# Kernel tuning notes

Hardware: AMD Instinct MI355X
Metric: run time of the kernel (lower is better)

Reference implementation:

```python
import jax, jax.numpy as jnp
import numpy as np

K = 1024          # num_embeddings
D = 256           # embedding_dim
BETA = 0.25       # commitment_cost
DECAY = 0.99
EPS = 1e-05
N = 65536         # number of tokens


def setup_inputs() -> dict:
    key = jax.random.key(0)
    k1, k2, k3 = jax.random.split(key, 3)
    inputs = jax.random.normal(k1, (N, D), dtype=jnp.float32)
    # codebook initialized uniform(-1/K, 1/K) as in torch init
    codebook = jax.random.uniform(k2, (K, D), dtype=jnp.float32, minval=-1.0 / K, maxval=1.0 / K)
    ema_cluster_size = jnp.zeros((K,), dtype=jnp.float32)
    ema_w = codebook  # _ema_w initialized to a clone of the weights
    return {"inputs": inputs, "codebook": codebook,
            "ema_cluster_size": ema_cluster_size, "ema_w": ema_w}


def reference(inputs, codebook, ema_cluster_size, ema_w):
    flat = inputs.reshape(-1, D)  # [N, D]
    # squared L2 distances to every codebook entry: [N, K]
    distances = (jnp.sum(flat * flat, axis=1, keepdims=True)
                 + jnp.sum(codebook * codebook, axis=1)
                 - 2.0 * jnp.matmul(flat, codebook.T))
    encoding_indices = jnp.argmin(distances, axis=1)          # [N]
    quantized = codebook[encoding_indices].reshape(inputs.shape)  # gather

    # EMA codebook update (training branch). one-hot^T @ flat == segment_sum.
    counts = jax.ops.segment_sum(jnp.ones((flat.shape[0],), flat.dtype),
                                 encoding_indices, num_segments=K)  # [K]
    dw = jax.ops.segment_sum(flat, encoding_indices, num_segments=K)  # [K, D]
    new_cs = DECAY * ema_cluster_size + (1.0 - DECAY) * counts
    n_total = jnp.sum(new_cs)
    new_cs = (new_cs + EPS) / (n_total + K * EPS) * n_total
    new_ema_w = DECAY * ema_w + (1.0 - DECAY) * dw
    new_weight = new_ema_w / new_cs[:, None]

    commitment_loss = jnp.mean((quantized - inputs) ** 2)
    vq_loss = BETA * commitment_loss
    quantized_st = inputs + jax.lax.stop_gradient(quantized - inputs)

    avg_probs = counts / flat.shape[0]
    perplexity = jnp.exp(-jnp.sum(avg_probs * jnp.log(avg_probs + 1e-10)))

    return (quantized_st, vq_loss, encoding_indices, perplexity,
            new_cs, new_ema_w, new_weight)
```

## Files before the change

kernel.cpp:

```cpp
#include <hip/hip_runtime.h>
#include <math.h>

#define KC 1024
#define DD 256
#define NT 65536
#define MARGIN 2.5e-4f
#define HCAP 4096

#define W_COUNTS 0
#define W_LOSS   1024
#define W_HCNT   1025
#define W_CNORM  1028
#define W_OFFS   2052
#define W_CUR    3076
#define W_HLIST  4100
#define W_SORT   8196
#define W_IDX    73732
#define W_DWB    139268
#define W_AMIN   401412
#define W_CCAT   409604
#define W_CBT    540676
#define W_XH     802820

typedef _Float16 h8 __attribute__((ext_vector_type(8)));
typedef _Float16 h4 __attribute__((ext_vector_type(4)));
typedef float f32x4 __attribute__((ext_vector_type(4)));
typedef unsigned long long u64;

__device__ __forceinline__ void gl_lds16(const _Float16* g, _Float16* l) {
    __builtin_amdgcn_global_load_lds(
        (const __attribute__((address_space(1))) unsigned int*)g,
        (__attribute__((address_space(3))) unsigned int*)l, 16, 0, 0);
}

__device__ __forceinline__ void merge2(float& v1, float& i1, float& v2,
                                       float b1, float bi, float b2) {
    if (b1 < v1) { v2 = fminf(v1, b2); v1 = b1; i1 = bi; }
    else         { v2 = fminf(v2, b1); }
}

__device__ __forceinline__ int physrow(int row, int d) {
    return ((((row >> 2) ^ ((d >> 2) & 7)) << 2) | (row & 3));
}

__global__ __launch_bounds__(256) void vq_prepx(const float* __restrict__ X,
                                                _Float16* __restrict__ Xcat) {
    int gid = blockIdx.x * 256 + threadIdx.x;
    float4 v = reinterpret_cast<const float4*>(X)[gid];
    int n = gid >> 6, d = (gid & 63) << 2;
    h4 hi;
    hi[0] = (_Float16)v.x; hi[1] = (_Float16)v.y;
    hi[2] = (_Float16)v.z; hi[3] = (_Float16)v.w;
    *(h4*)(Xcat + (size_t)n * 256 + d) = hi;
}

__global__ __launch_bounds__(64) void vq_prep(const float* __restrict__ cb,
                                              _Float16* __restrict__ Ccat,
                                              float* __restrict__ cnorm,
                                              float* __restrict__ cbT) {
    const int k = blockIdx.x;
    const int l = threadIdx.x;
    float4 v = reinterpret_cast<const float4*>(cb)[k * 64 + l];
    cbT[(4 * l + 0) * KC + k] = v.x;
    cbT[(4 * l + 1) * KC + k] = v.y;
    cbT[(4 * l + 2) * KC + k] = v.z;
    cbT[(4 * l + 3) * KC + k] = v.w;
    h4 hi;
    hi[0] = (_Float16)(v.x * 16384.0f); hi[1] = (_Float16)(v.y * 16384.0f);
    hi[2] = (_Float16)(v.z * 16384.0f); hi[3] = (_Float16)(v.w * 16384.0f);
    *(h4*)(Ccat + (size_t)k * 256 + 4 * l) = hi;
    float s = v.x * v.x + v.y * v.y + v.z * v.z + v.w * v.w;
    #pragma unroll
    for (int off = 32; off; off >>= 1) s += __shfl_down(s, off, 64);
    if (l == 0) cnorm[k] = s;
}

__global__ __launch_bounds__(256) void vq_screen(
        const _Float16* __restrict__ Xcat, const _Float16* __restrict__ Ccat,
        const float* __restrict__ cnorm, float* __restrict__ counts,
        int* __restrict__ idxw, float* __restrict__ idxf,
        int* __restrict__ hardCnt, int* __restrict__ hardList) {
    __shared__ _Float16 As[8192];
    __shared__ _Float16 Bs[8192];
    __shared__ float wbuf[2][128][3];
    const int t = threadIdx.x;
    const int lane = t & 63, w = t >> 6;
    const int wm0 = (w & 1) * 64, wn0 = (w >> 1) * 64;
    const int row0 = blockIdx.x * 128;

    int sA[4], mA[4], kgA[4];
    #pragma unroll
    for (int c = 0; c < 4; ++c) {
        int s = (w * 4 + c) * 64 + lane;
        sA[c] = s; mA[c] = s >> 3;
        kgA[c] = (((s & 7) ^ ((s >> 3) & 7)) << 3);
    }

    float rv1[16], ri1[16], rv2[16];
    #pragma unroll
    for (int i = 0; i < 16; ++i) { rv1[i] = 3.4e38f; ri1[i] = 0.f; rv2[i] = 3.4e38f; }

    for (int ct = 0; ct < 8; ++ct) {
        const int cb0 = ct * 128;
        f32x4 acc[4][4];
        #pragma unroll
        for (int i = 0; i < 4; ++i)
            #pragma unroll
            for (int j = 0; j < 4; ++j) acc[i][j] = {0.f, 0.f, 0.f, 0.f};

        for (int dk = 0; dk < 4; ++dk) {
            const int kk = dk * 64;
            __syncthreads();
            #pragma unroll
            for (int c = 0; c < 4; ++c) {
                gl_lds16(Xcat + (size_t)(row0 + mA[c]) * 256 + kk + kgA[c], As + sA[c] * 8);
                gl_lds16(Ccat + (size_t)(cb0  + mA[c]) * 256 + kk + kgA[c], Bs + sA[c] * 8);
            }
            __syncthreads();
            #pragma unroll
            for (int ks = 0; ks < 2; ++ks) {
                h8 av[4], bv[4];
                const int kg = ks * 4 + (lane >> 4);
                #pragma unroll
                for (int f = 0; f < 4; ++f) {
                    int ma = wm0 + f * 16 + (lane & 15);
                    av[f] = *(const h8*)(As + ma * 64 + ((kg ^ (ma & 7)) << 3));
                    int nb = wn0 + f * 16 + (lane & 15);
                    bv[f] = *(const h8*)(Bs + nb * 64 + ((kg ^ (nb & 7)) << 3));
                }
                #pragma unroll
                for (int i = 0; i < 4; ++i)
                    #pragma unroll
                    for (int j = 0; j < 4; ++j)
                        acc[i][j] = __builtin_amdgcn_mfma_f32_16x16x32_f16(
                            av[i], bv[j], acc[i][j], 0, 0, 0);
            }
        }
        float cnv[4]; float gnf[4];
        #pragma unroll
        for (int fj = 0; fj < 4; ++fj) {
            int gn = cb0 + wn0 + fj * 16 + (lane & 15);
            gnf[fj] = (float)gn; cnv[fj] = cnorm[gn];
        }
        #pragma unroll
        for (int fi = 0; fi < 4; ++fi) {
            #pragma unroll
            for (int r = 0; r < 4; ++r) {
                const int ix = fi * 4 + r;
                #pragma unroll
                for (int fj = 0; fj < 4; ++fj) {
                    float q = fmaf(acc[fi][fj][r], -1.220703125e-4f, cnv[fj]);
                    merge2(rv1[ix], ri1[ix], rv2[ix], q, gnf[fj], 3.4e38f);
                }
            }
        }
    }
    #pragma unroll
    for (int fi = 0; fi < 4; ++fi) {
        #pragma unroll
        for (int r = 0; r < 4; ++r) {
            const int ix = fi * 4 + r;
            float v1 = rv1[ix], i1 = ri1[ix], v2 = rv2[ix];
            #pragma unroll
            for (int msk = 1; msk <= 8; msk <<= 1) {
                float b1 = __shfl_xor(v1, msk, 64);
                float bi = __shfl_xor(i1, msk, 64);
                float b2 = __shfl_xor(v2, msk, 64);
                merge2(v1, i1, v2, b1, bi, b2);
            }
            if ((lane & 15) == 0) {
                int row = wm0 + fi * 16 + (lane >> 4) * 4 + r;
                wbuf[w >> 1][row][0] = v1;
                wbuf[w >> 1][row][1] = i1;
                wbuf[w >> 1][row][2] = v2;
            }
        }
    }
    __syncthreads();
    if (t < 128) {
        float v1 = wbuf[0][t][0], i1 = wbuf[0][t][1], v2 = wbuf[0][t][2];
        merge2(v1, i1, v2, wbuf[1][t][0], wbuf[1][t][1], wbuf[1][t][2]);
        int i1i = (int)i1;
        int n = row0 + t;
        idxf[n] = i1; idxw[n] = i1i;
        if (v2 - v1 > MARGIN) {
            unsafeAtomicAdd(&counts[i1i], 1.0f);
        } else {
            int p = atomicAdd(hardCnt, 1);
            if (p < HCAP) hardList[p] = n;
            else unsafeAtomicAdd(&counts[i1i], 1.0f);
        }
    }
}

__global__ __launch_bounds__(256) void vq_compact(const float* __restrict__ X,
                                                  const int* __restrict__ hardCnt,
                                                  const int* __restrict__ hardList,
                                                  float* __restrict__ Xh) {
    const int cnt = min(*hardCnt, HCAP);
    const int i = blockIdx.x * 4 + (threadIdx.x >> 6);
    const int lane = threadIdx.x & 63;
    float4 v = {0.f, 0.f, 0.f, 0.f};
    if (i < cnt) v = ((const float4*)(X + (size_t)hardList[i] * 256))[lane];
    ((float4*)(Xh + (size_t)i * 256))[lane] = v;
}

__global__ __launch_bounds__(256) void vq_exact(const float* __restrict__ Xh,
                                                const float* __restrict__ cbT,
                                                const float* __restrict__ cnorm,
                                                const int* __restrict__ hardCnt,
                                                u64* __restrict__ amin) {
    extern __shared__ float smem[];
    float* As = smem;
    float* Bs = smem + 32768;
    float* xn = smem + 36992 - 128;
    const int cnt = min(*hardCnt, HCAP);
    const int row0 = blockIdx.x * 128;
    if (row0 >= cnt) return;
    const int ct = blockIdx.y;
    const int t  = threadIdx.x;
    const int tx = t & 15;
    const int ty = t >> 4;

    const float4* X4 = reinterpret_cast<const float4*>(Xh);
    #pragma unroll 4
    for (int p = 0; p < 32; ++p) {
        int fid = p * 256 + t;
        int row = fid >> 6;
        int d4  = fid & 63;
        float4 v = X4[(size_t)row0 * 64 + (size_t)row * 64 + d4];
        int d = d4 << 2;
        int ph = physrow(row, d);
        As[(d + 0) * 128 + ph] = v.x;
        As[(d + 1) * 128 + ph] = v.y;
        As[(d + 2) * 128 + ph] = v.z;
        As[(d + 3) * 128 + ph] = v.w;
    }
    __syncthreads();

    if (t < 128) {
        #pragma clang fp contract(off)
        float tot = 0.f;
        #pragma unroll
        for (int h = 0; h < 2; ++h) {
            float r[8];
            #pragma unroll
            for (int j = 0; j < 8; ++j) {
                int d = h * 128 + j;
                float a = As[d * 128 + physrow(t, d)];
                float p = a * a;
                r[j] = p;
            }
            for (int i = 1; i < 16; ++i) {
                #pragma unroll
                for (int j = 0; j < 8; ++j) {
                    int d = h * 128 + i * 8 + j;
                    float a = As[d * 128 + physrow(t, d)];
                    float p = a * a;
                    r[j] = r[j] + p;
                }
            }
            float s = ((r[0] + r[1]) + (r[2] + r[3])) + ((r[4] + r[5]) + (r[6] + r[7]));
            tot = tot + s;
        }
        xn[t] = tot;
    }

    float acc[8][8];
    #pragma unroll
    for (int i = 0; i < 8; ++i)
        #pragma unroll
        for (int j = 0; j < 8; ++j) acc[i][j] = 0.f;

    const float4* cbT4 = reinterpret_cast<const float4*>(cbT);

    #pragma unroll 1
    for (int dk = 0; dk < 8; ++dk) {
        __syncthreads();
        #pragma unroll
        for (int it = 0; it < 4; ++it) {
            int fid = it * 256 + t;
            int dd  = fid >> 5;
            int c4  = fid & 31;
            float4 v = cbT4[(size_t)(dk * 32 + dd) * 256 + ct * 32 + c4];
            reinterpret_cast<float4*>(Bs)[dd * 32 + c4] = v;
        }
        __syncthreads();

        #pragma unroll 8
        for (int dd = 0; dd < 32; ++dd) {
            const int d  = dk * 32 + dd;
            const int sw = (dd >> 2) & 7;
            const int ar = ((ty ^ sw) << 2);
            const float4 a0 = *reinterpret_cast<const float4*>(&As[d * 128 + ar]);
            const float4 a1 = *reinterpret_cast<const float4*>(&As[d * 128 + ar + 64]);
            const float4 b0 = *reinterpret_cast<const float4*>(&Bs[dd * 128 + (tx << 2)]);
            const float4 b1 = *reinterpret_cast<const float4*>(&Bs[dd * 128 + (tx << 2) + 64]);
            const float av[8] = {a0.x, a0.y, a0.z, a0.w, a1.x, a1.y, a1.z, a1.w};
            const float bv[8] = {b0.x, b0.y, b0.z, b0.w, b1.x, b1.y, b1.z, b1.w};
            #pragma unroll
            for (int i = 0; i < 8; ++i)
                #pragma unroll
                for (int j = 0; j < 8; ++j)
                    acc[i][j] = fmaf(av[i], bv[j], acc[i][j]);
        }
    }

    u64 emin[8];
    #pragma unroll
    for (int i = 0; i < 8; ++i) emin[i] = ~0ull;
    {
        #pragma clang fp contract(off)
        float cnv[8];
        int   gcl[8];
        #pragma unroll
        for (int j = 0; j < 8; ++j) {
            int cl = (j < 4) ? (tx * 4 + j) : (64 + tx * 4 + (j - 4));
            gcl[j] = ct * 128 + cl;
            cnv[j] = cnorm[gcl[j]];
        }
        #pragma unroll
        for (int i = 0; i < 8; ++i) {
            int rowl = (i < 4) ? (ty * 4 + i) : (64 + ty * 4 + (i - 4));
            float xr = xn[rowl];
            #pragma unroll
            for (int j = 0; j < 8; ++j) {
                float t1 = xr + cnv[j];
                float t2 = 2.0f * acc[i][j];
                float s  = t1 - t2;
                u64 enc = ((u64)__float_as_uint(s) << 32) | (unsigned int)gcl[j];
                if (enc < emin[i]) emin[i] = enc;
            }
        }
    }
    __syncthreads();
    u64* red = reinterpret_cast<u64*>(Bs);
    #pragma unroll
    for (int i = 0; i < 8; ++i) {
        int rowl = (i < 4) ? (ty * 4 + i) : (64 + ty * 4 + (i - 4));
        red[rowl * 16 + tx] = emin[i];
    }
    __syncthreads();
    if (t < 128) {
        u64 m = ~0ull;
        #pragma unroll
        for (int x = 0; x < 16; ++x) m = min(m, red[t * 16 + x]);
        atomicMin(&amin[row0 + t], m);
    }
}

__global__ __launch_bounds__(256) void vq_fixup(const int* __restrict__ hardCnt,
                                                const int* __restrict__ hardList,
                                                const u64* __restrict__ amin,
                                                float* __restrict__ counts,
                                                int* __restrict__ idxw,
                                                float* __restrict__ idxf) {
    const int cnt = min(*hardCnt, HCAP);
    int i = blockIdx.x * 256 + threadIdx.x;
    if (i >= cnt) return;
    int tok = hardList[i];
    int code = (int)(amin[i] & 0xFFFFFFFFull);
    idxf[tok] = (float)code;
    idxw[tok] = code;
    unsafeAtomicAdd(&counts[code], 1.0f);
}

__global__ __launch_bounds__(1024) void vq_scan(const float* __restrict__ counts,
                                                int* __restrict__ offs,
                                                int* __restrict__ cursor) {
    __shared__ int sc[1024];
    const int t = threadIdx.x;
    int c = (int)counts[t];
    sc[t] = c;
    __syncthreads();
    #pragma unroll
    for (int off = 1; off < 1024; off <<= 1) {
        int v = (t >= off) ? sc[t - off] : 0;
        __syncthreads();
        sc[t] += v;
        __syncthreads();
    }
    int excl = sc[t] - c;
    offs[t] = excl;
    cursor[t] = excl;
}

__global__ __launch_bounds__(256) void vq_scatter(const int* __restrict__ idxw,
                                                  int* __restrict__ cursor,
                                                  int* __restrict__ sorted) {
    int n = blockIdx.x * 256 + threadIdx.x;
    int idx = idxw[n];
    int pos = atomicAdd(&cursor[idx], 1);
    sorted[pos] = n;
}

__global__ __launch_bounds__(256) void vq_dw(const float* __restrict__ X,
                                             const int* __restrict__ offs,
                                             const float* __restrict__ counts,
                                             const int* __restrict__ sorted,
                                             float* __restrict__ dw) {
    const int k = blockIdx.x;
    const int t = threadIdx.x;
    const int begin = offs[k];
    const int cnt = (int)counts[k];
    const int* seg = sorted + begin;
    float acc = 0.f;
    int i = 0;
    for (; i + 4 <= cnt; i += 4) {
        int t0 = seg[i], t1 = seg[i + 1], t2 = seg[i + 2], t3 = seg[i + 3];
        float a = X[(size_t)t0 * 256 + t];
        float b = X[(size_t)t1 * 256 + t];
        float c = X[(size_t)t2 * 256 + t];
        float d = X[(size_t)t3 * 256 + t];
        acc += a; acc += b; acc += c; acc += d;
    }
    for (; i < cnt; ++i) acc += X[(size_t)seg[i] * 256 + t];
    dw[k * 256 + t] = acc;
}

__global__ __launch_bounds__(256) void vq_out0(const float* __restrict__ X,
                                               const float* __restrict__ CB,
                                               const int* __restrict__ idxw,
                                               float* __restrict__ out0,
                                               float* __restrict__ loss) {
    const int t    = threadIdx.x;
    const int wave = (blockIdx.x * 256 + t) >> 6;
    const int lane = t & 63;
    const float4* X4 = reinterpret_cast<const float4*>(X);
    const float4* C4 = reinterpret_cast<const float4*>(CB);
    float4* O4 = reinterpret_cast<float4*>(out0);
    float lsum = 0.f;
    for (int r = 0; r < 64; ++r) {
        const int n = wave * 64 + r;
        const int idx = idxw[n];
        float4 x = X4[n * 64 + lane];
        float4 c = C4[idx * 64 + lane];
        float d0 = c.x - x.x, d1 = c.y - x.y, d2 = c.z - x.z, d3 = c.w - x.w;
        float4 q;
        q.x = x.x + d0; q.y = x.y + d1; q.z = x.z + d2; q.w = x.w + d3;
        O4[n * 64 + lane] = q;
        lsum += d0 * d0 + d1 * d1 + d2 * d2 + d3 * d3;
    }
    #pragma unroll
    for (int off = 32; off; off >>= 1) lsum += __shfl_down(lsum, off, 64);
    if (lane == 0) unsafeAtomicAdd(loss, lsum);
}

__global__ void vq_fin1(const float* __restrict__ counts,
                        const float* __restrict__ ecs,
                        const float* __restrict__ loss,
                        float* __restrict__ out1, float* __restrict__ out3,
                        float* __restrict__ out4) {
    __shared__ float sd[1024];
    const int t = threadIdx.x;
    float c   = counts[t];
    float pre = 0.99f * ecs[t] + 0.01f * c;
    sd[t] = pre; __syncthreads();
    for (int off = 512; off; off >>= 1) { if (t < off) sd[t] += sd[t + off]; __syncthreads(); }
    float n_total = sd[0];
    __syncthreads();
    float avg = c * (1.0f / 65536.0f);
    float ent = avg * logf(avg + 1e-10f);
    sd[t] = ent; __syncthreads();
    for (int off = 512; off; off >>= 1) { if (t < off) sd[t] += sd[t + off]; __syncthreads(); }
    float entsum = sd[0];
    float ncs = (pre + 1e-5f) / (n_total + 1024.0f * 1e-5f) * n_total;
    out4[t] = ncs;
    if (t == 0) {
        out1[0] = 0.25f * (loss[0] / 16777216.0f);
        out3[0] = expf(-entsum);
    }
}

__global__ __launch_bounds__(256) void vq_fin2(const float* __restrict__ emw,
                                               const float* __restrict__ dwv,
                                               const float* __restrict__ ncs,
                                               float* __restrict__ out5,
                                               float* __restrict__ out6) {
    int i = blockIdx.x * 256 + threadIdx.x;
    float e = 0.99f * emw[i] + 0.01f * dwv[i];
    out5[i] = e;
    out6[i] = e / ncs[i >> 8];
}

extern "C" void kernel_launch(void* const* d_in, const int* in_sizes, int n_in,
                              void* d_out, int out_size, void* d_ws, size_t ws_size,
                              hipStream_t stream) {
    const float* X   = (const float*)d_in[0];
    const float* CB  = (const float*)d_in[1];
    const float* ECS = (const float*)d_in[2];
    const float* EMW = (const float*)d_in[3];

    float* out0 = (float*)d_out;
    float* out1 = out0 + (size_t)NT * DD;
    float* out2 = out1 + 1;
    float* out3 = out2 + NT;
    float* out4 = out3 + 1;
    float* out5 = out4 + KC;
    float* out6 = out5 + (size_t)KC * DD;

    float* ws       = (float*)d_ws;
    float* counts   = ws + W_COUNTS;
    float* loss     = ws + W_LOSS;
    int*   hardCnt  = (int*)(ws + W_HCNT);
    float* cnorm    = ws + W_CNORM;
    int*   offs     = (int*)(ws + W_OFFS);
    int*   cursor   = (int*)(ws + W_CUR);
    int*   hardList = (int*)(ws + W_HLIST);
    int*   sorted   = (int*)(ws + W_SORT);
    int*   idxw     = (int*)(ws + W_IDX);
    float* dw       = ws + W_DWB;
    u64*   amin     = (u64*)(ws + W_AMIN);
    _Float16* Ccat  = (_Float16*)(ws + W_CCAT);
    float* cbT      = ws + W_CBT;
    float* Xh       = ws + W_XH;

    _Float16* Xcat = (_Float16*)d_out;

    (void)hipMemsetAsync(ws, 0, 1026 * sizeof(float), stream);
    (void)hipMemsetAsync(amin, 0xFF, (size_t)HCAP * 8, stream);

    vq_prepx<<<NT * DD / 4 / 256, 256, 0, stream>>>(X, Xcat);
    vq_prep<<<KC, 64, 0, stream>>>(CB, Ccat, cnorm, cbT);
    vq_screen<<<NT / 128, 256, 0, stream>>>(Xcat, Ccat, cnorm, counts, idxw, out2,
                                            hardCnt, hardList);
    vq_compact<<<HCAP / 4, 256, 0, stream>>>(X, hardCnt, hardList, Xh);
    vq_exact<<<dim3(HCAP / 128, 8), 256, 36992 * sizeof(float), stream>>>(
        Xh, cbT, cnorm, hardCnt, amin);
    vq_fixup<<<HCAP / 256, 256, 0, stream>>>(hardCnt, hardList, amin, counts,
                                             idxw, out2);
    vq_scan<<<1, 1024, 0, stream>>>(counts, offs, cursor);
    vq_scatter<<<NT / 256, 256, 0, stream>>>(idxw, cursor, sorted);
    vq_dw<<<KC, 256, 0, stream>>>(X, offs, counts, sorted, dw);
    vq_out0<<<256, 256, 0, stream>>>(X, CB, idxw, out0, loss);
    vq_fin1<<<1, 1024, 0, stream>>>(counts, ECS, loss, out1, out3, out4);
    vq_fin2<<<KC * DD / 256, 256, 0, stream>>>(EMW, dw, out4, out5, out6);
}
```

Measured before the change: 398.3 us.

## Keep input tile resident in LDS and double-buffer codebook tiles in vq_screen

The screening GEMM now loads the block's full 128x256 fp16 input tile into LDS once, instead of reloading it for each of the 8 codebook tiles. Codebook tiles are streamed in 128-dim halves into two LDS buffers. The next half is prefetched while MFMAs run on the current one, leaving one barrier per iteration instead of two per k-step. The cost is about 128KB of LDS per block and launch bounds of one block per CU. That cuts occupancy and the latency hiding it gave, against less global traffic and fewer syncs.

```diff
diff --git a/kernel.cpp b/kernel.cpp
--- a/kernel.cpp
+++ b/kernel.cpp
@@ -75,86 +75,110 @@
     if (l == 0) cnorm[k] = s;
 }
 
-__global__ __launch_bounds__(256) void vq_screen(
+__global__ __launch_bounds__(256, 1) void vq_screen(
         const _Float16* __restrict__ Xcat, const _Float16* __restrict__ Ccat,
         const float* __restrict__ cnorm, float* __restrict__ counts,
         int* __restrict__ idxw, float* __restrict__ idxf,
         int* __restrict__ hardCnt, int* __restrict__ hardList) {
-    __shared__ _Float16 As[8192];
-    __shared__ _Float16 Bs[8192];
+    __shared__ _Float16 As[32768];
+    __shared__ _Float16 Bs[2][16384];
     __shared__ float wbuf[2][128][3];
     const int t = threadIdx.x;
     const int lane = t & 63, w = t >> 6;
     const int wm0 = (w & 1) * 64, wn0 = (w >> 1) * 64;
     const int row0 = blockIdx.x * 128;
 
-    int sA[4], mA[4], kgA[4];
-    #pragma unroll
-    for (int c = 0; c < 4; ++c) {
-        int s = (w * 4 + c) * 64 + lane;
-        sA[c] = s; mA[c] = s >> 3;
-        kgA[c] = (((s & 7) ^ ((s >> 3) & 7)) << 3);
-    }
+    #pragma unroll
+    for (int r = 0; r < 16; ++r) {
+        int s = r * 256 + t;
+        int row = s >> 5, gp = s & 31;
+        int gl = gp ^ (row & 7);
+        gl_lds16(Xcat + (size_t)(row0 + row) * 256 + gl * 8, As + s * 8);
+    }
+    {
+        #pragma unroll
+        for (int r = 0; r < 8; ++r) {
+            int s = r * 256 + t;
+            int code = s >> 4, gp = s & 15;
+            int gl = gp ^ (code & 7);
+            gl_lds16(Ccat + (size_t)code * 256 + gl * 8, Bs[0] + s * 8);
+        }
+    }
+    __syncthreads();
 
     float rv1[16], ri1[16], rv2[16];
     #pragma unroll
     for (int i = 0; i < 16; ++i) { rv1[i] = 3.4e38f; ri1[i] = 0.f; rv2[i] = 3.4e38f; }
 
-    for (int ct = 0; ct < 8; ++ct) {
-        const int cb0 = ct * 128;
-        f32x4 acc[4][4];
-        #pragma unroll
-        for (int i = 0; i < 4; ++i)
-            #pragma unroll
-            for (int j = 0; j < 4; ++j) acc[i][j] = {0.f, 0.f, 0.f, 0.f};
-
-        for (int dk = 0; dk < 4; ++dk) {
-            const int kk = dk * 64;
-            __syncthreads();
-            #pragma unroll
-            for (int c = 0; c < 4; ++c) {
-                gl_lds16(Xcat + (size_t)(row0 + mA[c]) * 256 + kk + kgA[c], As + sA[c] * 8);
-                gl_lds16(Ccat + (size_t)(cb0  + mA[c]) * 256 + kk + kgA[c], Bs + sA[c] * 8);
-            }
-            __syncthreads();
-            #pragma unroll
-            for (int ks = 0; ks < 2; ++ks) {
-                h8 av[4], bv[4];
-                const int kg = ks * 4 + (lane >> 4);
+    f32x4 acc[4][4];
+
+    #pragma unroll 1
+    for (int it = 0; it < 16; ++it) {
+        const int ct = it >> 1, c = it & 1;
+        if (it + 1 < 16) {
+            const int jn = it + 1;
+            const int cb0n = (jn >> 1) * 128;
+            const int khn  = (jn & 1) * 128;
+            _Float16* Bn = Bs[jn & 1];
+            #pragma unroll
+            for (int r = 0; r < 8; ++r) {
+                int s = r * 256 + t;
+                int code = s >> 4, gp = s & 15;
+                int gl = gp ^ (code & 7);
+                gl_lds16(Ccat + (size_t)(cb0n + code) * 256 + khn + gl * 8,
+                         Bn + s * 8);
+            }
+        }
+        if (c == 0) {
+            #pragma unroll
+            for (int i = 0; i < 4; ++i)
                 #pragma unroll
-                for (int f = 0; f < 4; ++f) {
-                    int ma = wm0 + f * 16 + (lane & 15);
-                    av[f] = *(const h8*)(As + ma * 64 + ((kg ^ (ma & 7)) << 3));
-                    int nb = wn0 + f * 16 + (lane & 15);
-                    bv[f] = *(const h8*)(Bs + nb * 64 + ((kg ^ (nb & 7)) << 3));
+                for (int j = 0; j < 4; ++j) acc[i][j] = {0.f, 0.f, 0.f, 0.f};
+        }
+        const _Float16* Bc = Bs[it & 1];
+        #pragma unroll
+        for (int ks = 0; ks < 4; ++ks) {
+            h8 av[4], bv[4];
+            const int kq = ks * 4 + (lane >> 4);
+            const int kg = c * 16 + kq;
+            #pragma unroll
+            for (int f = 0; f < 4; ++f) {
+                int ma = wm0 + f * 16 + (lane & 15);
+                av[f] = *(const h8*)(As + ma * 256 + ((kg ^ (ma & 7)) << 3));
+                int nb = wn0 + f * 16 + (lane & 15);
+                bv[f] = *(const h8*)(Bc + nb * 128 + ((kq ^ (nb & 7)) << 3));
+            }
+            #pragma unroll
+            for (int i = 0; i < 4; ++i)
+                #pragma unroll
+                for (int j = 0; j < 4; ++j)
+                    acc[i][j] = __builtin_amdgcn_mfma_f32_16x16x32_f16(
+                        av[i], bv[j], acc[i][j], 0, 0, 0);
+        }
+        if (c == 1) {
+            const int cb0 = ct * 128;
+            float cnv[4]; float gnf[4];
+            #pragma unroll
+            for (int fj = 0; fj < 4; ++fj) {
+                int gn = cb0 + wn0 + fj * 16 + (lane & 15);
+                gnf[fj] = (float)gn; cnv[fj] = cnorm[gn];
+            }
+            #pragma unroll
+            for (int fi = 0; fi < 4; ++fi) {
+                #pragma unroll
+                for (int r = 0; r < 4; ++r) {
+                    const int ix = fi * 4 + r;
+                    #pragma unroll
+                    for (int fj = 0; fj < 4; ++fj) {
+                        float q = fmaf(acc[fi][fj][r], -1.220703125e-4f, cnv[fj]);
+                        merge2(rv1[ix], ri1[ix], rv2[ix], q, gnf[fj], 3.4e38f);
+                    }
                 }
-                #pragma unroll
-                for (int i = 0; i < 4; ++i)
-                    #pragma unroll
-                    for (int j = 0; j < 4; ++j)
-                        acc[i][j] = __builtin_amdgcn_mfma_f32_16x16x32_f16(
-                            av[i], bv[j], acc[i][j], 0, 0, 0);
-            }
-        }
-        float cnv[4]; float gnf[4];
-        #pragma unroll
-        for (int fj = 0; fj < 4; ++fj) {
-            int gn = cb0 + wn0 + fj * 16 + (lane & 15);
-            gnf[fj] = (float)gn; cnv[fj] = cnorm[gn];
-        }
-        #pragma unroll
-        for (int fi = 0; fi < 4; ++fi) {
-            #pragma unroll
-            for (int r = 0; r < 4; ++r) {
-                const int ix = fi * 4 + r;
-                #pragma unroll
-                for (int fj = 0; fj < 4; ++fj) {
-                    float q = fmaf(acc[fi][fj][r], -1.220703125e-4f, cnv[fj]);
-                    merge2(rv1[ix], ri1[ix], rv2[ix], q, gnf[fj], 3.4e38f);
-                }
-            }
-        }
-    }
+            }
+        }
+        __syncthreads();
+    }
+
     #pragma unroll
     for (int fi = 0; fi < 4; ++fi) {
         #pragma unroll
```

Result: no change. 395.7 us (-0.6%).

## Keep full X tile resident in LDS and read pre-swizzled codebook fragments directly

Applied to the files above, without the earlier changes.

The screening GEMM now loads the whole 128x256 fp16 X tile into shared memory once per block instead of restaging X and codebook tiles for every K-step and codebook chunk. The codebook is written by the prep kernel in an MFMA-fragment-ordered layout, so each lane reads its B operand straight from global or L2 as one 16-byte load with no shared-memory staging and no per-step barriers. The aim is to cut repeated X reloads and synchronisation inside the main loop. In exchange, B operands now come from global memory with latency that is not hidden by staging, and the 64KB LDS tile plus launch_bounds(256,2) may limit occupancy and register headroom.

```diff
diff --git a/kernel.cpp b/kernel.cpp
--- a/kernel.cpp
+++ b/kernel.cpp
@@ -55,7 +55,7 @@
 }
 
 __global__ __launch_bounds__(64) void vq_prep(const float* __restrict__ cb,
-                                              _Float16* __restrict__ Ccat,
+                                              _Float16* __restrict__ Cfrag,
                                               float* __restrict__ cnorm,
                                               float* __restrict__ cbT) {
     const int k = blockIdx.x;
@@ -68,78 +68,78 @@
     h4 hi;
     hi[0] = (_Float16)(v.x * 16384.0f); hi[1] = (_Float16)(v.y * 16384.0f);
     hi[2] = (_Float16)(v.z * 16384.0f); hi[3] = (_Float16)(v.w * 16384.0f);
-    *(h4*)(Ccat + (size_t)k * 256 + 4 * l) = hi;
+    {
+        const int d  = 4 * l;
+        const int tc = k >> 4;
+        const int ks = d >> 5;
+        const int ln = ((d >> 3) & 3) * 16 + (k & 15);
+        const int gran = (tc * 8 + ks) * 64 + ln;
+        *(h4*)(Cfrag + (size_t)gran * 8 + (d & 7)) = hi;
+    }
     float s = v.x * v.x + v.y * v.y + v.z * v.z + v.w * v.w;
     #pragma unroll
     for (int off = 32; off; off >>= 1) s += __shfl_down(s, off, 64);
     if (l == 0) cnorm[k] = s;
 }
 
-__global__ __launch_bounds__(256) void vq_screen(
-        const _Float16* __restrict__ Xcat, const _Float16* __restrict__ Ccat,
+__global__ __launch_bounds__(256, 2) void vq_screen(
+        const _Float16* __restrict__ Xcat, const _Float16* __restrict__ Cfrag,
         const float* __restrict__ cnorm, float* __restrict__ counts,
         int* __restrict__ idxw, float* __restrict__ idxf,
         int* __restrict__ hardCnt, int* __restrict__ hardList) {
-    __shared__ _Float16 As[8192];
-    __shared__ _Float16 Bs[8192];
+    __shared__ _Float16 As[32768];
     __shared__ float wbuf[2][128][3];
     const int t = threadIdx.x;
     const int lane = t & 63, w = t >> 6;
-    const int wm0 = (w & 1) * 64, wn0 = (w >> 1) * 64;
+    const int wm0 = (w & 1) * 64, wn0q = (w >> 1) * 4;
     const int row0 = blockIdx.x * 128;
 
-    int sA[4], mA[4], kgA[4];
-    #pragma unroll
-    for (int c = 0; c < 4; ++c) {
-        int s = (w * 4 + c) * 64 + lane;
-        sA[c] = s; mA[c] = s >> 3;
-        kgA[c] = (((s & 7) ^ ((s >> 3) & 7)) << 3);
-    }
+    #pragma unroll
+    for (int r = 0; r < 16; ++r) {
+        int s = r * 256 + t;
+        int row = s >> 5, gp = s & 31;
+        int gl = gp ^ (row & 7);
+        gl_lds16(Xcat + (size_t)(row0 + row) * 256 + gl * 8, As + s * 8);
+    }
+    __syncthreads();
 
     float rv1[16], ri1[16], rv2[16];
     #pragma unroll
     for (int i = 0; i < 16; ++i) { rv1[i] = 3.4e38f; ri1[i] = 0.f; rv2[i] = 3.4e38f; }
 
+    const h8* Cf8 = (const h8*)Cfrag;
+
+    #pragma unroll 1
     for (int ct = 0; ct < 8; ++ct) {
-        const int cb0 = ct * 128;
         f32x4 acc[4][4];
         #pragma unroll
         for (int i = 0; i < 4; ++i)
             #pragma unroll
             for (int j = 0; j < 4; ++j) acc[i][j] = {0.f, 0.f, 0.f, 0.f};
 
-        for (int dk = 0; dk < 4; ++dk) {
-            const int kk = dk * 64;
-            __syncthreads();
-            #pragma unroll
-            for (int c = 0; c < 4; ++c) {
-                gl_lds16(Xcat + (size_t)(row0 + mA[c]) * 256 + kk + kgA[c], As + sA[c] * 8);
-                gl_lds16(Ccat + (size_t)(cb0  + mA[c]) * 256 + kk + kgA[c], Bs + sA[c] * 8);
-            }
-            __syncthreads();
-            #pragma unroll
-            for (int ks = 0; ks < 2; ++ks) {
-                h8 av[4], bv[4];
-                const int kg = ks * 4 + (lane >> 4);
+        #pragma unroll
+        for (int ks = 0; ks < 8; ++ks) {
+            h8 av[4], bv[4];
+            const int kg = ks * 4 + (lane >> 4);
+            #pragma unroll
+            for (int f = 0; f < 4; ++f) {
+                int ma = wm0 + f * 16 + (lane & 15);
+                av[f] = *(const h8*)(As + ma * 256 + ((kg ^ (ma & 7)) << 3));
+                int tc = ct * 8 + wn0q + f;
+                bv[f] = Cf8[(tc * 8 + ks) * 64 + lane];
+            }
+            #pragma unroll
+            for (int i = 0; i < 4; ++i)
                 #pragma unroll
-                for (int f = 0; f < 4; ++f) {
-                    int ma = wm0 + f * 16 + (lane & 15);
-                    av[f] = *(const h8*)(As + ma * 64 + ((kg ^ (ma & 7)) << 3));
-                    int nb = wn0 + f * 16 + (lane & 15);
-                    bv[f] = *(const h8*)(Bs + nb * 64 + ((kg ^ (nb & 7)) << 3));
-                }
-                #pragma unroll
-                for (int i = 0; i < 4; ++i)
-                    #pragma unroll
-                    for (int j = 0; j < 4; ++j)
-                        acc[i][j] = __builtin_amdgcn_mfma_f32_16x16x32_f16(
-                            av[i], bv[j], acc[i][j], 0, 0, 0);
-            }
-        }
+                for (int j = 0; j < 4; ++j)
+                    acc[i][j] = __builtin_amdgcn_mfma_f32_16x16x32_f16(
+                        av[i], bv[j], acc[i][j], 0, 0, 0);
+        }
+        const int cb0 = ct * 128 + wn0q * 16;
         float cnv[4]; float gnf[4];
         #pragma unroll
         for (int fj = 0; fj < 4; ++fj) {
-            int gn = cb0 + wn0 + fj * 16 + (lane & 15);
+            int gn = cb0 + fj * 16 + (lane & 15);
             gnf[fj] = (float)gn; cnv[fj] = cnorm[gn];
         }
         #pragma unroll
@@ -155,6 +155,7 @@
             }
         }
     }
+
     #pragma unroll
     for (int fi = 0; fi < 4; ++fi) {
         #pragma unroll
@@ -511,7 +512,7 @@
     int*   idxw     = (int*)(ws + W_IDX);
     float* dw       = ws + W_DWB;
     u64*   amin     = (u64*)(ws + W_AMIN);
-    _Float16* Ccat  = (_Float16*)(ws + W_CCAT);
+    _Float16* Cfrag = (_Float16*)(ws + W_CCAT);
     float* cbT      = ws + W_CBT;
     float* Xh       = ws + W_XH;
 
@@ -521,8 +522,8 @@
     (void)hipMemsetAsync(amin, 0xFF, (size_t)HCAP * 8, stream);
 
     vq_prepx<<<NT * DD / 4 / 256, 256, 0, stream>>>(X, Xcat);
-    vq_prep<<<KC, 64, 0, stream>>>(CB, Ccat, cnorm, cbT);
-    vq_screen<<<NT / 128, 256, 0, stream>>>(Xcat, Ccat, cnorm, counts, idxw, out2,
+    vq_prep<<<KC, 64, 0, stream>>>(CB, Cfrag, cnorm, cbT);
+    vq_screen<<<NT / 128, 256, 0, stream>>>(Xcat, Cfrag, cnorm, counts, idxw, out2,
                                             hardCnt, hardList);
     vq_compact<<<HCAP / 4, 256, 0, stream>>>(X, hardCnt, hardList, Xh);
     vq_exact<<<dim3(HCAP / 128, 8), 256, 36992 * sizeof(float), stream>>>(
```

Result: no change. 397.4 us (-0.2%).
